# Kernel optimization log

Measured on AMD Instinct MI355X. Metric: run time of the kernel, lower is better.

Reference implementation:

```python
import jax, jax.numpy as jnp
import numpy as np

UNFOLDS = 6
DELTA_T = 0.1
TAU = 1.0


def setup_inputs() -> dict:
    key = jax.random.key(0)
    k1, k2, k3 = jax.random.split(key, 3)
    B, D, N = 8192, 512, 512
    inputs = jax.random.normal(k1, (B, D), dtype=jnp.float32)
    state = jax.random.normal(k2, (B, N), dtype=jnp.float32)
    # xavier_uniform for W of shape (fan_in=D+N, fan_out=N)
    fan_in, fan_out = D + N, N
    limit = float(np.sqrt(6.0 / (fan_in + fan_out)))
    W = jax.random.uniform(k3, (fan_in, fan_out), dtype=jnp.float32,
                           minval=-limit, maxval=limit)
    bias = jnp.zeros((N,), dtype=jnp.float32)
    return {"inputs": inputs, "state": state, "W": W, "bias": bias}


def reference(inputs, state, W, bias):
    # CTRNN Euler integration with global feedback, fix_tau=True, cell_clip=0.
    # Each unfold: fused = [inputs, state]; f = tanh(fused @ W + b);
    # state += dt * (-state/tau + f)
    for _ in range(UNFOLDS):  # fixed small unroll count (6)
        fused = jnp.concatenate([inputs, state], axis=-1)  # (B, D+N)
        input_f_prime = jnp.tanh(fused @ W + bias)          # (B, N)
        state = state + DELTA_T * (-state / TAU + input_f_prime)
    return (state, state)
```

## Files before the change

### kernel.cpp

```cpp
#include <hip/hip_runtime.h>
#include <hip/hip_bf16.h>


#define BB 8192
#define DD 512
#define NN 512
#define BM 32
#define NTHREADS 512
#define NUNFOLD 6

using f32x4 = __attribute__((ext_vector_type(4))) float;
using i32x4 = __attribute__((ext_vector_type(4))) int;
typedef unsigned int u32;

#define WLIMIT 0.0625f
#define SW_INV (127.0f / WLIMIT)
#define SA_INV (127.0f / 6.0f)
#define QSCALE ((WLIMIT / 127.0f) * (6.0f / 127.0f))
#define EXP2S  2.8853900817779268f
#define QS2    (QSCALE * EXP2S)

__device__ __forceinline__ unsigned short f2bf(float f) {
    unsigned int u = __float_as_uint(f);
    u += 0x7fffu + ((u >> 16) & 1u);
    return (unsigned short)(u >> 16);
}
__device__ __forceinline__ int f2q(float f, float scale) {
    float q = rintf(f * scale);
    q = fminf(fmaxf(q, -127.f), 127.f);
    return (int)q;
}
__device__ __forceinline__ int f2qf(float f, float scale) {
    return (int)rintf(f * scale);
}

__global__ void w_quant(const float* __restrict__ W,
                        signed char* __restrict__ WQ) {
    int c    = blockIdx.x * blockDim.x + threadIdx.x;
    int lane = c & 63;
    int nt   = (c >> 6) & 3;
    int g    = (c >> 8) & 15;
    int wv   = c >> 12;
    int n  = (wv * 4 + nt) * 16 + (lane & 15);
    int k0 = g * 64 + (lane >> 4) * 16;
    signed char v[16];
#pragma unroll
    for (int e = 0; e < 16; ++e)
        v[e] = (signed char)f2q(W[(size_t)(k0 + e) * NN + n], SW_INV);
    *reinterpret_cast<i32x4*>(WQ + (size_t)c * 16) =
        *reinterpret_cast<const i32x4*>(v);
}

__global__ __launch_bounds__(NTHREADS)
void ctrnn_fused(const float* __restrict__ inputs,
                 const float* __restrict__ state,
                 const float* __restrict__ bias,
                 const signed char* __restrict__ WQ,
                 float* __restrict__ out) {
    __shared__ __align__(16) char Alds[2][32 * 512];
    __shared__ __align__(16) char Wlds[8][4][4096];

    const int tid  = threadIdx.x;
    const int lane = tid & 63;
    const int wv   = tid >> 6;
    const int row0 = blockIdx.x * BM;
    const int l15  = lane & 15;
    const int l4   = lane >> 4;
    const int rot8 = (blockIdx.x >> 3) & 7;
    const int rot4 = rot8 & 3;

    const char* wq = (const char*)WQ + (size_t)wv * 65536 + (size_t)lane * 16;

    auto ldA = [&](int buf, int mt, int off) -> i32x4 {
        int r = mt * 16 + l15;
        int byte = (r * 512 + off) ^ ((r & 7) << 4);
        return *reinterpret_cast<const i32x4*>(&Alds[buf][byte]);
    };

    i32x4 acc[2][4];

    {
        const float4* s4 = reinterpret_cast<const float4*>(inputs + (size_t)row0 * DD);
#pragma unroll
        for (int i = 0; i < 2; ++i) {
            int qc = tid + i * NTHREADS;
            int r = qc >> 5, c16 = qc & 31;
            u32 w[4];
#pragma unroll
            for (int m = 0; m < 4; ++m) {
                float4 v = s4[qc * 4 + m];
                w[m] = ((u32)(unsigned char)(signed char)f2qf(v.x, SA_INV)) |
                       ((u32)(unsigned char)(signed char)f2qf(v.y, SA_INV) << 8) |
                       ((u32)(unsigned char)(signed char)f2qf(v.z, SA_INV) << 16) |
                       ((u32)(unsigned char)(signed char)f2qf(v.w, SA_INV) << 24);
            }
            int byte = (r * 512 + c16 * 16) ^ ((r & 7) << 4);
            *reinterpret_cast<uint4*>(&Alds[0][byte]) = *reinterpret_cast<const uint4*>(w);
        }
#pragma unroll
        for (int gs = 0; gs < 4; ++gs)
#pragma unroll
            for (int nt = 0; nt < 4; ++nt) {
                i32x4 v = *reinterpret_cast<const i32x4*>(
                    wq + (size_t)(8 + gs) * 4096 + nt * 1024);
                *reinterpret_cast<i32x4*>(&Wlds[wv][gs][nt * 1024 + lane * 16]) = v;
            }
    }

    f32x4 sreg[2][4];
#pragma unroll
    for (int mt = 0; mt < 2; ++mt)
#pragma unroll
        for (int nt = 0; nt < 4; ++nt)
#pragma unroll
            for (int j = 0; j < 4; ++j)
                sreg[mt][nt][j] =
                    state[(size_t)(row0 + mt * 16 + l4 * 4 + j) * NN +
                          (wv * 64 + nt * 16 + l15)];

    __syncthreads();

#pragma unroll
    for (int mt = 0; mt < 2; ++mt)
#pragma unroll
        for (int nt = 0; nt < 4; ++nt)
            acc[mt][nt] = i32x4{0, 0, 0, 0};
    {
        i32x4 bA[4], bB[4];
        auto lg = [&](i32x4 (&b)[4], int g) {
#pragma unroll
            for (int nt = 0; nt < 4; ++nt)
                b[nt] = *reinterpret_cast<const i32x4*>(
                    wq + (size_t)g * 4096 + nt * 1024);
        };
        auto cs = [&](i32x4 (&b)[4], int g) {
            int off = g * 64 + l4 * 16;
            i32x4 a0 = ldA(0, 0, off);
            i32x4 a1 = ldA(0, 1, off);
#pragma unroll
            for (int nt = 0; nt < 4; ++nt) {
                acc[0][nt] = __builtin_amdgcn_mfma_i32_16x16x64_i8(
                    a0, b[nt], acc[0][nt], 0, 0, 0);
                acc[1][nt] = __builtin_amdgcn_mfma_i32_16x16x64_i8(
                    a1, b[nt], acc[1][nt], 0, 0, 0);
            }
        };
        lg(bA, rot8);
        lg(bB, (rot8 + 1) & 7);
#pragma unroll
        for (int gp = 0; gp < 4; ++gp) {
            cs(bA, (rot8 + 2 * gp) & 7);
            if (gp < 3) lg(bA, (rot8 + 2 * gp + 2) & 7);
            cs(bB, (rot8 + 2 * gp + 1) & 7);
            if (gp < 3) lg(bB, (rot8 + 2 * gp + 3) & 7);
        }
    }

    u32 projp[2][4][2];
#pragma unroll
    for (int nt = 0; nt < 4; ++nt) {
        float bv = EXP2S * bias[wv * 64 + nt * 16 + l15];
#pragma unroll
        for (int mt = 0; mt < 2; ++mt)
#pragma unroll
            for (int p = 0; p < 2; ++p) {
                float v0 = QS2 * (float)acc[mt][nt][2 * p] + bv;
                float v1 = QS2 * (float)acc[mt][nt][2 * p + 1] + bv;
                projp[mt][nt][p] = (u32)f2bf(v0) | ((u32)f2bf(v1) << 16);
            }
    }

#pragma unroll
    for (int mt = 0; mt < 2; ++mt)
#pragma unroll
        for (int nt = 0; nt < 4; ++nt)
#pragma unroll
            for (int j = 0; j < 4; ++j) {
                int r = mt * 16 + l4 * 4 + j;
                int c = wv * 64 + nt * 16 + l15;
                Alds[1][(r * 512 + c) ^ ((r & 7) << 4)] =
                    (char)(signed char)f2qf(sreg[mt][nt][j], SA_INV);
            }
    __syncthreads();

    const int s0 = 4 + ((0 + rot4) & 3);
    const int s1 = 4 + ((1 + rot4) & 3);
    const int s2 = 4 + ((2 + rot4) & 3);
    const int s3 = 4 + ((3 + rot4) & 3);

#pragma unroll 1
    for (int u = 0; u < NUNFOLD; ++u) {
        const int rb = (u & 1) ^ 1;
        const int wb = u & 1;
#pragma unroll
        for (int mt = 0; mt < 2; ++mt)
#pragma unroll
            for (int nt = 0; nt < 4; ++nt)
                acc[mt][nt] = i32x4{0, 0, 0, 0};

        i32x4 bA[4], bB[4];
        auto lg = [&](i32x4 (&b)[4], int gk) {
#pragma unroll
            for (int nt = 0; nt < 4; ++nt)
                b[nt] = *reinterpret_cast<const i32x4*>(
                    wq + (size_t)(8 + gk) * 4096 + nt * 1024);
        };
        auto cs = [&](i32x4 (&b)[4], int gk) {
            int off = gk * 64 + l4 * 16;
            i32x4 a0 = ldA(rb, 0, off);
            i32x4 a1 = ldA(rb, 1, off);
#pragma unroll
            for (int nt = 0; nt < 4; ++nt) {
                acc[0][nt] = __builtin_amdgcn_mfma_i32_16x16x64_i8(
                    a0, b[nt], acc[0][nt], 0, 0, 0);
                acc[1][nt] = __builtin_amdgcn_mfma_i32_16x16x64_i8(
                    a1, b[nt], acc[1][nt], 0, 0, 0);
            }
        };
        auto cl = [&](int gs) {
            int off = gs * 64 + l4 * 16;
            i32x4 a0 = ldA(rb, 0, off);
            i32x4 a1 = ldA(rb, 1, off);
#pragma unroll
            for (int nt = 0; nt < 4; ++nt) {
                i32x4 w = *reinterpret_cast<const i32x4*>(
                    &Wlds[wv][gs][nt * 1024 + lane * 16]);
                acc[0][nt] = __builtin_amdgcn_mfma_i32_16x16x64_i8(
                    a0, w, acc[0][nt], 0, 0, 0);
                acc[1][nt] = __builtin_amdgcn_mfma_i32_16x16x64_i8(
                    a1, w, acc[1][nt], 0, 0, 0);
            }
        };

        lg(bA, s0); lg(bB, s1);
        cl(0);
        cs(bA, s0); lg(bA, s2);
        cl(1);
        cs(bB, s1); lg(bB, s3);
        cl(2);
        cs(bA, s2);
        cl(3);
        cs(bB, s3);

#pragma unroll
        for (int mt = 0; mt < 2; ++mt)
#pragma unroll
            for (int nt = 0; nt < 4; ++nt)
#pragma unroll
                for (int j = 0; j < 4; ++j) {
                    u32 pr = projp[mt][nt][j >> 1];
                    float pj = (j & 1) ? __uint_as_float(pr & 0xffff0000u)
                                       : __uint_as_float(pr << 16);
                    float e2 = fmaf(QS2, (float)acc[mt][nt][j], pj);
                    float e  = exp2f(e2);
                    float rc = __builtin_amdgcn_rcpf(e + 1.f);
                    float s = fmaf(-0.2f, rc, fmaf(sreg[mt][nt][j], 0.9f, 0.1f));
                    sreg[mt][nt][j] = s;
                    int r = mt * 16 + l4 * 4 + j;
                    int c = wv * 64 + nt * 16 + l15;
                    Alds[wb][(r * 512 + c) ^ ((r & 7) << 4)] =
                        (char)(signed char)f2qf(s, SA_INV);
                }
        __syncthreads();
    }

#pragma unroll
    for (int mt = 0; mt < 2; ++mt)
#pragma unroll
        for (int nt = 0; nt < 4; ++nt)
#pragma unroll
            for (int j = 0; j < 4; ++j) {
                size_t r = (size_t)(row0 + mt * 16 + l4 * 4 + j);
                int c = wv * 64 + nt * 16 + l15;
                float s = sreg[mt][nt][j];
                out[r * NN + c] = s;
                out[(size_t)BB * NN + r * NN + c] = s;
            }
}

extern "C" void kernel_launch(void* const* d_in, const int* in_sizes, int n_in,
                              void* d_out, int out_size, void* d_ws, size_t ws_size,
                              hipStream_t stream) {
    const float* inputs = (const float*)d_in[0];
    const float* state  = (const float*)d_in[1];
    const float* W      = (const float*)d_in[2];
    const float* bias   = (const float*)d_in[3];
    float* out = (float*)d_out;
    signed char* WQ = (signed char*)d_ws;

    w_quant<<<32768 / 512, 512, 0, stream>>>(W, WQ);
    ctrnn_fused<<<BB / BM, NTHREADS, 0, stream>>>(inputs, state, bias, WQ, out);
}
```

Measured before the change: 44.51 us.

## Remap waves to 2x4 row/column tiling with 128-column weight slices

Measured after the change: 61.52 us. +38.2%, slower.

```diff
diff --git a/kernel.cpp b/kernel.cpp
--- a/kernel.cpp
+++ b/kernel.cpp
@@ -38,10 +38,10 @@
                         signed char* __restrict__ WQ) {
     int c    = blockIdx.x * blockDim.x + threadIdx.x;
     int lane = c & 63;
-    int nt   = (c >> 6) & 3;
-    int g    = (c >> 8) & 15;
-    int wv   = c >> 12;
-    int n  = (wv * 4 + nt) * 16 + (lane & 15);
+    int nt   = (c >> 6) & 7;
+    int g    = (c >> 9) & 15;
+    int wc   = c >> 13;
+    int n  = wc * 128 + nt * 16 + (lane & 15);
     int k0 = g * 64 + (lane >> 4) * 16;
     signed char v[16];
 #pragma unroll
@@ -58,26 +58,28 @@
                  const signed char* __restrict__ WQ,
                  float* __restrict__ out) {
     __shared__ __align__(16) char Alds[2][32 * 512];
-    __shared__ __align__(16) char Wlds[8][4][4096];
+    __shared__ __align__(16) char Wlds[4][4][8192];
 
     const int tid  = threadIdx.x;
     const int lane = tid & 63;
     const int wv   = tid >> 6;
+    const int wr   = wv >> 2;
+    const int wc   = wv & 3;
     const int row0 = blockIdx.x * BM;
     const int l15  = lane & 15;
     const int l4   = lane >> 4;
     const int rot8 = (blockIdx.x >> 3) & 7;
     const int rot4 = rot8 & 3;
 
-    const char* wq = (const char*)WQ + (size_t)wv * 65536 + (size_t)lane * 16;
-
-    auto ldA = [&](int buf, int mt, int off) -> i32x4 {
-        int r = mt * 16 + l15;
+    const char* wq = (const char*)WQ + (size_t)wc * 131072 + (size_t)lane * 16;
+
+    auto ldA = [&](int buf, int off) -> i32x4 {
+        int r = wr * 16 + l15;
         int byte = (r * 512 + off) ^ ((r & 7) << 4);
         return *reinterpret_cast<const i32x4*>(&Alds[buf][byte]);
     };
 
-    i32x4 acc[2][4];
+    i32x4 acc8[8];
 
     {
         const float4* s4 = reinterpret_cast<const float4*>(inputs + (size_t)row0 * DD);
@@ -97,185 +99,158 @@
             int byte = (r * 512 + c16 * 16) ^ ((r & 7) << 4);
             *reinterpret_cast<uint4*>(&Alds[0][byte]) = *reinterpret_cast<const uint4*>(w);
         }
-#pragma unroll
-        for (int gs = 0; gs < 4; ++gs)
-#pragma unroll
-            for (int nt = 0; nt < 4; ++nt) {
-                i32x4 v = *reinterpret_cast<const i32x4*>(
-                    wq + (size_t)(8 + gs) * 4096 + nt * 1024);
-                *reinterpret_cast<i32x4*>(&Wlds[wv][gs][nt * 1024 + lane * 16]) = v;
-            }
-    }
-
-    f32x4 sreg[2][4];
-#pragma unroll
-    for (int mt = 0; mt < 2; ++mt)
-#pragma unroll
-        for (int nt = 0; nt < 4; ++nt)
-#pragma unroll
-            for (int j = 0; j < 4; ++j)
-                sreg[mt][nt][j] =
-                    state[(size_t)(row0 + mt * 16 + l4 * 4 + j) * NN +
-                          (wv * 64 + nt * 16 + l15)];
+        if (wr == 0) {
+#pragma unroll
+            for (int gs = 0; gs < 4; ++gs)
+#pragma unroll
+                for (int nt = 0; nt < 8; ++nt)
+                    *reinterpret_cast<i32x4*>(&Wlds[wc][gs][nt * 1024 + lane * 16]) =
+                        *reinterpret_cast<const i32x4*>(
+                            wq + (size_t)(8 + gs) * 8192 + nt * 1024);
+        }
+    }
+
+    f32x4 sreg[8];
+#pragma unroll
+    for (int nt = 0; nt < 8; ++nt)
+#pragma unroll
+        for (int j = 0; j < 4; ++j)
+            sreg[nt][j] = state[(size_t)(row0 + wr * 16 + l4 * 4 + j) * NN +
+                                (wc * 128 + nt * 16 + l15)];
 
     __syncthreads();
 
 #pragma unroll
-    for (int mt = 0; mt < 2; ++mt)
-#pragma unroll
-        for (int nt = 0; nt < 4; ++nt)
-            acc[mt][nt] = i32x4{0, 0, 0, 0};
+    for (int nt = 0; nt < 8; ++nt)
+        acc8[nt] = i32x4{0, 0, 0, 0};
     {
         i32x4 bA[4], bB[4];
-        auto lg = [&](i32x4 (&b)[4], int g) {
-#pragma unroll
-            for (int nt = 0; nt < 4; ++nt)
-                b[nt] = *reinterpret_cast<const i32x4*>(
-                    wq + (size_t)g * 4096 + nt * 1024);
-        };
-        auto cs = [&](i32x4 (&b)[4], int g) {
-            int off = g * 64 + l4 * 16;
-            i32x4 a0 = ldA(0, 0, off);
-            i32x4 a1 = ldA(0, 1, off);
-#pragma unroll
-            for (int nt = 0; nt < 4; ++nt) {
-                acc[0][nt] = __builtin_amdgcn_mfma_i32_16x16x64_i8(
-                    a0, b[nt], acc[0][nt], 0, 0, 0);
-                acc[1][nt] = __builtin_amdgcn_mfma_i32_16x16x64_i8(
-                    a1, b[nt], acc[1][nt], 0, 0, 0);
-            }
-        };
-        lg(bA, rot8);
-        lg(bB, (rot8 + 1) & 7);
-#pragma unroll
-        for (int gp = 0; gp < 4; ++gp) {
-            cs(bA, (rot8 + 2 * gp) & 7);
-            if (gp < 3) lg(bA, (rot8 + 2 * gp + 2) & 7);
-            cs(bB, (rot8 + 2 * gp + 1) & 7);
-            if (gp < 3) lg(bB, (rot8 + 2 * gp + 3) & 7);
-        }
-    }
-
-    u32 projp[2][4][2];
-#pragma unroll
-    for (int nt = 0; nt < 4; ++nt) {
-        float bv = EXP2S * bias[wv * 64 + nt * 16 + l15];
-#pragma unroll
-        for (int mt = 0; mt < 2; ++mt)
-#pragma unroll
-            for (int p = 0; p < 2; ++p) {
-                float v0 = QS2 * (float)acc[mt][nt][2 * p] + bv;
-                float v1 = QS2 * (float)acc[mt][nt][2 * p + 1] + bv;
-                projp[mt][nt][p] = (u32)f2bf(v0) | ((u32)f2bf(v1) << 16);
-            }
-    }
-
-#pragma unroll
-    for (int mt = 0; mt < 2; ++mt)
-#pragma unroll
-        for (int nt = 0; nt < 4; ++nt)
-#pragma unroll
-            for (int j = 0; j < 4; ++j) {
-                int r = mt * 16 + l4 * 4 + j;
-                int c = wv * 64 + nt * 16 + l15;
-                Alds[1][(r * 512 + c) ^ ((r & 7) << 4)] =
-                    (char)(signed char)f2qf(sreg[mt][nt][j], SA_INV);
-            }
+        auto lgh = [&](i32x4 (&b)[4], int i) {
+            int g = (rot8 + (i >> 1)) & 7;
+            int h = i & 1;
+#pragma unroll
+            for (int n4 = 0; n4 < 4; ++n4)
+                b[n4] = *reinterpret_cast<const i32x4*>(
+                    wq + (size_t)g * 8192 + (h * 4 + n4) * 1024);
+        };
+        auto csh = [&](i32x4 (&b)[4], int i) {
+            int g = (rot8 + (i >> 1)) & 7;
+            int h = i & 1;
+            i32x4 a = ldA(0, g * 64 + l4 * 16);
+#pragma unroll
+            for (int n4 = 0; n4 < 4; ++n4)
+                acc8[h * 4 + n4] = __builtin_amdgcn_mfma_i32_16x16x64_i8(
+                    a, b[n4], acc8[h * 4 + n4], 0, 0, 0);
+        };
+        lgh(bA, 0);
+        lgh(bB, 1);
+#pragma unroll
+        for (int i = 0; i < 16; ++i) {
+            if (i & 1) { csh(bB, i); if (i < 14) lgh(bB, i + 2); }
+            else       { csh(bA, i); if (i < 14) lgh(bA, i + 2); }
+        }
+    }
+
+    u32 projp[8][2];
+#pragma unroll
+    for (int nt = 0; nt < 8; ++nt) {
+        float bv = EXP2S * bias[wc * 128 + nt * 16 + l15];
+#pragma unroll
+        for (int p = 0; p < 2; ++p) {
+            float v0 = QS2 * (float)acc8[nt][2 * p] + bv;
+            float v1 = QS2 * (float)acc8[nt][2 * p + 1] + bv;
+            projp[nt][p] = (u32)f2bf(v0) | ((u32)f2bf(v1) << 16);
+        }
+    }
+
+#pragma unroll
+    for (int nt = 0; nt < 8; ++nt)
+#pragma unroll
+        for (int j = 0; j < 4; ++j) {
+            int r = wr * 16 + l4 * 4 + j;
+            int c = wc * 128 + nt * 16 + l15;
+            Alds[1][(r * 512 + c) ^ ((r & 7) << 4)] =
+                (char)(signed char)f2qf(sreg[nt][j], SA_INV);
+        }
     __syncthreads();
-
-    const int s0 = 4 + ((0 + rot4) & 3);
-    const int s1 = 4 + ((1 + rot4) & 3);
-    const int s2 = 4 + ((2 + rot4) & 3);
-    const int s3 = 4 + ((3 + rot4) & 3);
 
 #pragma unroll 1
     for (int u = 0; u < NUNFOLD; ++u) {
         const int rb = (u & 1) ^ 1;
         const int wb = u & 1;
 #pragma unroll
-        for (int mt = 0; mt < 2; ++mt)
-#pragma unroll
-            for (int nt = 0; nt < 4; ++nt)
-                acc[mt][nt] = i32x4{0, 0, 0, 0};
+        for (int nt = 0; nt < 8; ++nt)
+            acc8[nt] = i32x4{0, 0, 0, 0};
 
         i32x4 bA[4], bB[4];
-        auto lg = [&](i32x4 (&b)[4], int gk) {
-#pragma unroll
-            for (int nt = 0; nt < 4; ++nt)
-                b[nt] = *reinterpret_cast<const i32x4*>(
-                    wq + (size_t)(8 + gk) * 4096 + nt * 1024);
-        };
-        auto cs = [&](i32x4 (&b)[4], int gk) {
-            int off = gk * 64 + l4 * 16;
-            i32x4 a0 = ldA(rb, 0, off);
-            i32x4 a1 = ldA(rb, 1, off);
-#pragma unroll
-            for (int nt = 0; nt < 4; ++nt) {
-                acc[0][nt] = __builtin_amdgcn_mfma_i32_16x16x64_i8(
-                    a0, b[nt], acc[0][nt], 0, 0, 0);
-                acc[1][nt] = __builtin_amdgcn_mfma_i32_16x16x64_i8(
-                    a1, b[nt], acc[1][nt], 0, 0, 0);
+        auto lgr = [&](i32x4 (&b)[4], int i) {
+            int gk = 4 + ((rot4 + (i >> 1)) & 3);
+            int h = i & 1;
+#pragma unroll
+            for (int n4 = 0; n4 < 4; ++n4)
+                b[n4] = *reinterpret_cast<const i32x4*>(
+                    wq + (size_t)(8 + gk) * 8192 + (h * 4 + n4) * 1024);
+        };
+        auto csr = [&](i32x4 (&b)[4], int i) {
+            int gk = 4 + ((rot4 + (i >> 1)) & 3);
+            int h = i & 1;
+            i32x4 a = ldA(rb, gk * 64 + l4 * 16);
+#pragma unroll
+            for (int n4 = 0; n4 < 4; ++n4)
+                acc8[h * 4 + n4] = __builtin_amdgcn_mfma_i32_16x16x64_i8(
+                    a, b[n4], acc8[h * 4 + n4], 0, 0, 0);
+        };
+        auto clr = [&](int gs, int h) {
+            i32x4 a = ldA(rb, gs * 64 + l4 * 16);
+#pragma unroll
+            for (int n4 = 0; n4 < 4; ++n4) {
+                i32x4 w = *reinterpret_cast<const i32x4*>(
+                    &Wlds[wc][gs][(h * 4 + n4) * 1024 + lane * 16]);
+                acc8[h * 4 + n4] = __builtin_amdgcn_mfma_i32_16x16x64_i8(
+                    a, w, acc8[h * 4 + n4], 0, 0, 0);
             }
         };
-        auto cl = [&](int gs) {
-            int off = gs * 64 + l4 * 16;
-            i32x4 a0 = ldA(rb, 0, off);
-            i32x4 a1 = ldA(rb, 1, off);
-#pragma unroll
-            for (int nt = 0; nt < 4; ++nt) {
-                i32x4 w = *reinterpret_cast<const i32x4*>(
-                    &Wlds[wv][gs][nt * 1024 + lane * 16]);
-                acc[0][nt] = __builtin_amdgcn_mfma_i32_16x16x64_i8(
-                    a0, w, acc[0][nt], 0, 0, 0);
-                acc[1][nt] = __builtin_amdgcn_mfma_i32_16x16x64_i8(
-                    a1, w, acc[1][nt], 0, 0, 0);
+
+        lgr(bA, 0); lgr(bB, 1);
+        clr(0, 0); csr(bA, 0); lgr(bA, 2);
+        clr(0, 1); csr(bB, 1); lgr(bB, 3);
+        clr(1, 0); csr(bA, 2); lgr(bA, 4);
+        clr(1, 1); csr(bB, 3); lgr(bB, 5);
+        clr(2, 0); csr(bA, 4); lgr(bA, 6);
+        clr(2, 1); csr(bB, 5); lgr(bB, 7);
+        clr(3, 0); csr(bA, 6);
+        clr(3, 1); csr(bB, 7);
+
+#pragma unroll
+        for (int nt = 0; nt < 8; ++nt)
+#pragma unroll
+            for (int j = 0; j < 4; ++j) {
+                u32 pr = projp[nt][j >> 1];
+                float pj = (j & 1) ? __uint_as_float(pr & 0xffff0000u)
+                                   : __uint_as_float(pr << 16);
+                float e2 = fmaf(QS2, (float)acc8[nt][j], pj);
+                float e  = exp2f(e2);
+                float rc = __builtin_amdgcn_rcpf(e + 1.f);
+                float s = fmaf(-0.2f, rc, fmaf(sreg[nt][j], 0.9f, 0.1f));
+                sreg[nt][j] = s;
+                int r = wr * 16 + l4 * 4 + j;
+                int c = wc * 128 + nt * 16 + l15;
+                Alds[wb][(r * 512 + c) ^ ((r & 7) << 4)] =
+                    (char)(signed char)f2qf(s, SA_INV);
             }
-        };
-
-        lg(bA, s0); lg(bB, s1);
-        cl(0);
-        cs(bA, s0); lg(bA, s2);
-        cl(1);
-        cs(bB, s1); lg(bB, s3);
-        cl(2);
-        cs(bA, s2);
-        cl(3);
-        cs(bB, s3);
-
-#pragma unroll
-        for (int mt = 0; mt < 2; ++mt)
-#pragma unroll
-            for (int nt = 0; nt < 4; ++nt)
-#pragma unroll
-                for (int j = 0; j < 4; ++j) {
-                    u32 pr = projp[mt][nt][j >> 1];
-                    float pj = (j & 1) ? __uint_as_float(pr & 0xffff0000u)
-                                       : __uint_as_float(pr << 16);
-                    float e2 = fmaf(QS2, (float)acc[mt][nt][j], pj);
-                    float e  = exp2f(e2);
-                    float rc = __builtin_amdgcn_rcpf(e + 1.f);
-                    float s = fmaf(-0.2f, rc, fmaf(sreg[mt][nt][j], 0.9f, 0.1f));
-                    sreg[mt][nt][j] = s;
-                    int r = mt * 16 + l4 * 4 + j;
-                    int c = wv * 64 + nt * 16 + l15;
-                    Alds[wb][(r * 512 + c) ^ ((r & 7) << 4)] =
-                        (char)(signed char)f2qf(s, SA_INV);
-                }
         __syncthreads();
     }
 
 #pragma unroll
-    for (int mt = 0; mt < 2; ++mt)
-#pragma unroll
-        for (int nt = 0; nt < 4; ++nt)
-#pragma unroll
-            for (int j = 0; j < 4; ++j) {
-                size_t r = (size_t)(row0 + mt * 16 + l4 * 4 + j);
-                int c = wv * 64 + nt * 16 + l15;
-                float s = sreg[mt][nt][j];
-                out[r * NN + c] = s;
-                out[(size_t)BB * NN + r * NN + c] = s;
-            }
+    for (int nt = 0; nt < 8; ++nt)
+#pragma unroll
+        for (int j = 0; j < 4; ++j) {
+            size_t r = (size_t)(row0 + wr * 16 + l4 * 4 + j);
+            int c = wc * 128 + nt * 16 + l15;
+            float s = sreg[nt][j];
+            out[r * NN + c] = s;
+            out[(size_t)BB * NN + r * NN + c] = s;
+        }
 }
 
 extern "C" void kernel_launch(void* const* d_in, const int* in_sizes, int n_in,
```
